# Performance work log

Hardware: AMD Instinct MI355X
Metric: run time of the kernel (lower is better)

## Reference

```python
import jax, jax.numpy as jnp
import numpy as np

B = 2048
H = 4096
K = 4  # conv kernel size


def setup_inputs() -> dict:
    key = jax.random.key(0)
    ks = jax.random.split(key, 9)
    s = 1.0 / np.sqrt(H)
    x = jax.random.normal(ks[0], (B, H), dtype=jnp.float32)
    conv_state = jax.random.normal(ks[1], (B, H, K - 1), dtype=jnp.float32)
    rglru_state = jax.random.normal(ks[2], (B, H), dtype=jnp.float32)
    w_fused = jax.random.uniform(ks[3], (2 * H, H), jnp.float32, -s, s)
    conv_w = jax.random.uniform(ks[4], (H, K), jnp.float32, -0.5, 0.5)
    conv_b = jax.random.uniform(ks[5], (H,), jnp.float32, -0.5, 0.5)
    w_gates = jax.random.uniform(ks[6], (2 * H, H), jnp.float32, -s, s)
    a = jax.random.uniform(ks[7], (H,), jnp.float32, 0.5, 0.9)
    w_out = jax.random.uniform(ks[8], (H, H), jnp.float32, -s, s)
    return {"x": x, "conv_state": conv_state, "rglru_state": rglru_state,
            "w_fused": w_fused, "conv_w": conv_w, "conv_b": conv_b,
            "w_gates": w_gates, "a": a, "w_out": w_out}


def reference(x, conv_state, rglru_state, w_fused, conv_w, conv_b, w_gates, a, w_out):
    # fused input projection -> gate branch + recurrent branch
    fused = x @ w_fused.T                       # [B, 2H]
    gate_out, x_recur = fused[:, :H], fused[:, H:]
    gate = jax.nn.gelu(gate_out, approximate=False)

    # single-step causal depthwise conv
    xws = jnp.concatenate([conv_state, x_recur[:, :, None]], axis=-1)  # [B, H, K]
    x_conv = jnp.einsum('bhk,hk->bh', xws, conv_w) + conv_b            # [B, H]
    new_conv_state = xws[:, :, 1:]                                     # [B, H, K-1]

    # RG-LRU gates
    gates = x_conv @ w_gates.T                  # [B, 2H]
    i_t = jax.nn.sigmoid(gates[:, :H])
    r_t = jax.nn.sigmoid(gates[:, H:])
    a_t = jnp.exp(8.0 * r_t * jnp.log(a))       # a ** (8 * r_t), a > 0
    multiplier = jnp.sqrt(1.0 - a_t * a_t)
    new_rglru_state = rglru_state * a_t + multiplier * (i_t * x_conv)

    out = (gate * new_rglru_state) @ w_out.T    # [B, H]
    return out, new_conv_state, new_rglru_state
```

## Files before the change

kernel.cpp:

```cpp
#include <hip/hip_runtime.h>
#include <cstdint>
#include <cstddef>

#define HD   4096
#define BSZ  2048

constexpr int BM = 128, BN = 128, BKT = 64;

typedef __bf16 bf16x8 __attribute__((ext_vector_type(8)));
typedef float  f32x4  __attribute__((ext_vector_type(4)));

__device__ __forceinline__ unsigned short f2bf(float f) {
  unsigned u = __float_as_uint(f);
  u += 0x7fffu + ((u >> 16) & 1u);
  return (unsigned short)(u >> 16);
}
__device__ __forceinline__ float bf2f(unsigned short s) {
  return __uint_as_float(((unsigned)s) << 16);
}

#define AS1(p) ((__attribute__((address_space(1))) void*)(void*)(p))
#define AS3(p) ((__attribute__((address_space(3))) void*)(p))

__global__ void cvt_f32_to_bf16(const float4* __restrict__ src,
                                ushort4* __restrict__ dst, int n4) {
  int i = blockIdx.x * blockDim.x + threadIdx.x;
  if (i >= n4) return;
  float4 v = src[i];
  ushort4 o;
  o.x = f2bf(v.x); o.y = f2bf(v.y); o.z = f2bf(v.z); o.w = f2bf(v.w);
  dst[i] = o;
}

template <int MODE>
__global__ __launch_bounds__(256) void gemm_bt(
    const unsigned short* __restrict__ A, const unsigned short* __restrict__ Bw,
    float* __restrict__ outf, unsigned short* __restrict__ gate_bf,
    float* __restrict__ xrec, int M, int N, int K) {
  __shared__ unsigned short smA[BM * BKT];
  __shared__ unsigned short smB[BN * BKT];
  const int tid  = threadIdx.x;
  const int wid  = tid >> 6;
  const int lane = tid & 63;
  const int wm = wid >> 1, wn = wid & 1;
  const int l16 = lane & 15, q = lane >> 4;
  const int bx = blockIdx.x, by = blockIdx.y;
  const int srow = tid >> 3;
  const int scol = (tid & 7) * 8;
  const unsigned short* Ab = A + (size_t)(by * BM) * K + scol;
  const unsigned short* Bb = Bw + (size_t)(bx * BN) * K + scol;
  const int ldsbase = (wid * 8) * BKT;
  f32x4 acc[4][4] = {};

  for (int kt = 0; kt < K; kt += BKT) {
#pragma unroll
    for (int i = 0; i < 4; ++i) {
      __builtin_amdgcn_global_load_lds(AS1(Ab + (size_t)(i * 32 + srow) * K + kt),
                                       AS3(smA + i * 32 * BKT + ldsbase), 16, 0, 0);
      __builtin_amdgcn_global_load_lds(AS1(Bb + (size_t)(i * 32 + srow) * K + kt),
                                       AS3(smB + i * 32 * BKT + ldsbase), 16, 0, 0);
    }
    __syncthreads();
#pragma unroll
    for (int kk = 0; kk < BKT; kk += 32) {
      bf16x8 af[4], bfr[4];
#pragma unroll
      for (int i = 0; i < 4; ++i)
        af[i]  = *(const bf16x8*)(smA + (wm * 64 + i * 16 + l16) * BKT + kk + q * 8);
#pragma unroll
      for (int j = 0; j < 4; ++j)
        bfr[j] = *(const bf16x8*)(smB + (wn * 64 + j * 16 + l16) * BKT + kk + q * 8);
#pragma unroll
      for (int i = 0; i < 4; ++i)
#pragma unroll
        for (int j = 0; j < 4; ++j)
          acc[i][j] = __builtin_amdgcn_mfma_f32_16x16x32_bf16(af[i], bfr[j], acc[i][j], 0, 0, 0);
    }
    __syncthreads();
  }

  const int gm0 = by * BM + wm * 64 + q * 4;
  const int gn0 = bx * BN + wn * 64 + l16;
#pragma unroll
  for (int i = 0; i < 4; ++i) {
#pragma unroll
    for (int j = 0; j < 4; ++j) {
      const int n = gn0 + j * 16;
#pragma unroll
      for (int r = 0; r < 4; ++r) {
        const int m = gm0 + i * 16 + r;
        float v = acc[i][j][r];
        if (MODE == 0) {
          outf[(size_t)m * N + n] = v;
        } else {
          if (n < HD) {
            float g = 0.5f * v * (1.0f + erff(v * 0.70710678118654752f));
            gate_bf[(size_t)m * HD + n] = f2bf(g);
          } else {
            xrec[(size_t)m * HD + (n - HD)] = v;
          }
        }
      }
    }
  }
}

__global__ void conv_fuse(const float* __restrict__ cs, const float* xr,
                          const float4* __restrict__ cw, const float* __restrict__ cb,
                          float* __restrict__ ncs, float* xc_out,
                          unsigned short* __restrict__ xc_bf) {
  int t = blockIdx.x * 256 + threadIdx.x;
  int h = t & (HD - 1);
  float c0 = cs[3 * t + 0];
  float c1 = cs[3 * t + 1];
  float c2 = cs[3 * t + 2];
  float xv = xr[t];
  float4 w = cw[h];
  float v = fmaf(c0, w.x, fmaf(c1, w.y, fmaf(c2, w.z, fmaf(xv, w.w, cb[h]))));
  ncs[3 * t + 0] = c1;
  ncs[3 * t + 1] = c2;
  ncs[3 * t + 2] = xv;
  xc_out[t] = v;
  xc_bf[t] = f2bf(v);
}

__global__ void rglru_fuse(const float* __restrict__ gates, const float* __restrict__ av,
                           const float* __restrict__ rs, const float* __restrict__ xc,
                           const unsigned short* __restrict__ gbf,
                           float* __restrict__ nrs, unsigned short* __restrict__ gated) {
  int t = blockIdx.x * 256 + threadIdx.x;
  int h = t & (HD - 1);
  int b = t >> 12;
  float gi = gates[(size_t)b * (2 * HD) + h];
  float gr = gates[(size_t)b * (2 * HD) + HD + h];
  float it = 1.0f / (1.0f + expf(-gi));
  float rt = 1.0f / (1.0f + expf(-gr));
  float at = expf(8.0f * rt * logf(av[h]));
  float mult = sqrtf(fmaxf(0.0f, 1.0f - at * at));
  float x = xc[t];
  float nv = fmaf(rs[t], at, mult * (it * x));
  nrs[t] = nv;
  gated[t] = f2bf(bf2f(gbf[t]) * nv);
}

extern "C" void kernel_launch(void* const* d_in, const int* in_sizes, int n_in,
                              void* d_out, int out_size, void* d_ws, size_t ws_size,
                              hipStream_t stream) {
  const float* x  = (const float*)d_in[0];
  const float* cs = (const float*)d_in[1];
  const float* rs = (const float*)d_in[2];
  const float* wf = (const float*)d_in[3];
  const float* cw = (const float*)d_in[4];
  const float* cb = (const float*)d_in[5];
  const float* wg = (const float*)d_in[6];
  const float* av = (const float*)d_in[7];
  const float* wo = (const float*)d_in[8];

  float* out = (float*)d_out;
  float* ncs = out + (size_t)BSZ * HD;
  float* nrs = out + (size_t)BSZ * HD * 4;

  char* ws = (char*)d_ws;
  unsigned short* x_bf   = (unsigned short*)(ws);
  unsigned short* wf_bf  = (unsigned short*)(ws + (size_t)(16u)  * 1048576u);
  unsigned short* wg_bf  = (unsigned short*)(ws + (size_t)(80u)  * 1048576u);
  unsigned short* wo_bf  = (unsigned short*)(ws + (size_t)(144u) * 1048576u);
  unsigned short* gatebf = (unsigned short*)(ws + (size_t)(176u) * 1048576u);
  float*          xrc    = (float*)         (ws + (size_t)(192u) * 1048576u);
  unsigned short* xc_bf  = (unsigned short*)(ws + (size_t)(224u) * 1048576u);
  float*          gates  = (float*)wf_bf;
  unsigned short* gated  = x_bf;

  cvt_f32_to_bf16<<<(BSZ * HD / 4) / 256, 256, 0, stream>>>((const float4*)x,  (ushort4*)x_bf,  BSZ * HD / 4);
  cvt_f32_to_bf16<<<(2 * HD * HD / 4) / 256, 256, 0, stream>>>((const float4*)wf, (ushort4*)wf_bf, 2 * HD * HD / 4);
  cvt_f32_to_bf16<<<(2 * HD * HD / 4) / 256, 256, 0, stream>>>((const float4*)wg, (ushort4*)wg_bf, 2 * HD * HD / 4);
  cvt_f32_to_bf16<<<(HD * HD / 4) / 256, 256, 0, stream>>>((const float4*)wo, (ushort4*)wo_bf, HD * HD / 4);

  dim3 blk(256);
  dim3 g1(2 * HD / BN, BSZ / BM);
  gemm_bt<1><<<g1, blk, 0, stream>>>(x_bf, wf_bf, nullptr, gatebf, xrc, BSZ, 2 * HD, HD);
  conv_fuse<<<(BSZ * HD) / 256, 256, 0, stream>>>(cs, xrc, (const float4*)cw, cb, ncs, xrc, xc_bf);
  gemm_bt<0><<<g1, blk, 0, stream>>>(xc_bf, wg_bf, gates, nullptr, nullptr, BSZ, 2 * HD, HD);
  rglru_fuse<<<(BSZ * HD) / 256, 256, 0, stream>>>(gates, av, rs, xrc, gatebf, nrs, gated);
  dim3 g3(HD / BN, BSZ / BM);
  gemm_bt<0><<<g3, blk, 0, stream>>>(gated, wo_bf, out, nullptr, nullptr, BSZ, HD, HD);
}
```

Measured before the change: 1.093 ms.

## XOR-swizzle GEMM LDS tiles and fuse sigmoid into gates GEMM epilogue

Applies an XOR swizzle to the 16-byte chunk column of the LDS A/B tiles, both when loading global-to-LDS and when reading fragments. With the old 128-byte row stride, 16 lanes reading the same column offset hit the same banks; the swizzle spreads those reads across banks. A new GEMM mode applies the sigmoid in the epilogue and writes bf16 gates. This halves the gates intermediate traffic and removes the exp from the elementwise kernel, at the cost of bf16 rounding on the gates.

```diff
diff --git a/kernel.cpp b/kernel.cpp
--- a/kernel.cpp
+++ b/kernel.cpp
@@ -46,7 +46,7 @@
   const int l16 = lane & 15, q = lane >> 4;
   const int bx = blockIdx.x, by = blockIdx.y;
   const int srow = tid >> 3;
-  const int scol = (tid & 7) * 8;
+  const int scol = (((tid & 7) ^ ((tid >> 3) & 7)) * 8);
   const unsigned short* Ab = A + (size_t)(by * BM) * K + scol;
   const unsigned short* Bb = Bw + (size_t)(bx * BN) * K + scol;
   const int ldsbase = (wid * 8) * BKT;
@@ -65,11 +65,15 @@
     for (int kk = 0; kk < BKT; kk += 32) {
       bf16x8 af[4], bfr[4];
 #pragma unroll
-      for (int i = 0; i < 4; ++i)
-        af[i]  = *(const bf16x8*)(smA + (wm * 64 + i * 16 + l16) * BKT + kk + q * 8);
+      for (int i = 0; i < 4; ++i) {
+        const int ar = wm * 64 + i * 16 + l16;
+        af[i]  = *(const bf16x8*)(smA + ar * BKT + ((((kk >> 3) + q) ^ (ar & 7)) * 8));
+      }
 #pragma unroll
-      for (int j = 0; j < 4; ++j)
-        bfr[j] = *(const bf16x8*)(smB + (wn * 64 + j * 16 + l16) * BKT + kk + q * 8);
+      for (int j = 0; j < 4; ++j) {
+        const int br = wn * 64 + j * 16 + l16;
+        bfr[j] = *(const bf16x8*)(smB + br * BKT + ((((kk >> 3) + q) ^ (br & 7)) * 8));
+      }
 #pragma unroll
       for (int i = 0; i < 4; ++i)
 #pragma unroll
@@ -92,6 +96,9 @@
         float v = acc[i][j][r];
         if (MODE == 0) {
           outf[(size_t)m * N + n] = v;
+        } else if (MODE == 2) {
+          float s = 1.0f / (1.0f + expf(-v));
+          gate_bf[(size_t)m * N + n] = f2bf(s);
         } else {
           if (n < HD) {
             float g = 0.5f * v * (1.0f + erff(v * 0.70710678118654752f));
@@ -124,17 +131,16 @@
   xc_bf[t] = f2bf(v);
 }
 
-__global__ void rglru_fuse(const float* __restrict__ gates, const float* __restrict__ av,
+__global__ void rglru_fuse(const unsigned short* __restrict__ gates_bf,
+                           const float* __restrict__ av,
                            const float* __restrict__ rs, const float* __restrict__ xc,
                            const unsigned short* __restrict__ gbf,
                            float* __restrict__ nrs, unsigned short* __restrict__ gated) {
   int t = blockIdx.x * 256 + threadIdx.x;
   int h = t & (HD - 1);
   int b = t >> 12;
-  float gi = gates[(size_t)b * (2 * HD) + h];
-  float gr = gates[(size_t)b * (2 * HD) + HD + h];
-  float it = 1.0f / (1.0f + expf(-gi));
-  float rt = 1.0f / (1.0f + expf(-gr));
+  float it = bf2f(gates_bf[(size_t)b * (2 * HD) + h]);
+  float rt = bf2f(gates_bf[(size_t)b * (2 * HD) + HD + h]);
   float at = expf(8.0f * rt * logf(av[h]));
   float mult = sqrtf(fmaxf(0.0f, 1.0f - at * at));
   float x = xc[t];
@@ -168,8 +174,8 @@
   unsigned short* gatebf = (unsigned short*)(ws + (size_t)(176u) * 1048576u);
   float*          xrc    = (float*)         (ws + (size_t)(192u) * 1048576u);
   unsigned short* xc_bf  = (unsigned short*)(ws + (size_t)(224u) * 1048576u);
-  float*          gates  = (float*)wf_bf;
-  unsigned short* gated  = x_bf;
+  unsigned short* gates_bf = wf_bf;
+  unsigned short* gated    = x_bf;
 
   cvt_f32_to_bf16<<<(BSZ * HD / 4) / 256, 256, 0, stream>>>((const float4*)x,  (ushort4*)x_bf,  BSZ * HD / 4);
   cvt_f32_to_bf16<<<(2 * HD * HD / 4) / 256, 256, 0, stream>>>((const float4*)wf, (ushort4*)wf_bf, 2 * HD * HD / 4);
@@ -180,8 +186,8 @@
   dim3 g1(2 * HD / BN, BSZ / BM);
   gemm_bt<1><<<g1, blk, 0, stream>>>(x_bf, wf_bf, nullptr, gatebf, xrc, BSZ, 2 * HD, HD);
   conv_fuse<<<(BSZ * HD) / 256, 256, 0, stream>>>(cs, xrc, (const float4*)cw, cb, ncs, xrc, xc_bf);
-  gemm_bt<0><<<g1, blk, 0, stream>>>(xc_bf, wg_bf, gates, nullptr, nullptr, BSZ, 2 * HD, HD);
-  rglru_fuse<<<(BSZ * HD) / 256, 256, 0, stream>>>(gates, av, rs, xrc, gatebf, nrs, gated);
+  gemm_bt<2><<<g1, blk, 0, stream>>>(xc_bf, wg_bf, nullptr, gates_bf, nullptr, BSZ, 2 * HD, HD);
+  rglru_fuse<<<(BSZ * HD) / 256, 256, 0, stream>>>(gates_bf, av, rs, xrc, gatebf, nrs, gated);
   dim3 g3(HD / BN, BSZ / BM);
   gemm_bt<0><<<g3, blk, 0, stream>>>(gated, wo_bf, out, nullptr, nullptr, BSZ, HD, HD);
 }
```

Result: faster. 1.002 ms (-8.3%).
